# Kernel optimization log

Measured on AMD Instinct MI355X. Metric: run time of the kernel, lower is better.

The kernel has to match this reference:

```python
import jax, jax.numpy as jnp
import numpy as np

HEADS = 4
DIM_HEAD = 32
DIM = 128
EPS = 1e-12  # F.normalize eps


def _rmsnorm(t, g):
    # F.normalize over channel dim (dim=1), then * g * sqrt(dim)
    n = jnp.sqrt(jnp.sum(t * t, axis=1, keepdims=True))
    return t / jnp.maximum(n, EPS) * g * (DIM ** 0.5)


def setup_inputs() -> dict:
    key = jax.random.key(0)
    ks = jax.random.split(key, 5)
    b, H, W = 16, 96, 96
    x = jax.random.normal(ks[0], (b, DIM, H, W), dtype=jnp.float32)
    norm_g = jnp.ones((1, DIM, 1, 1), dtype=jnp.float32)
    qkv_w = jax.random.normal(ks[1], (3 * HEADS * DIM_HEAD, DIM), dtype=jnp.float32) * 0.05
    mem_kv = jax.random.normal(ks[2], (2, HEADS, DIM_HEAD, 4), dtype=jnp.float32)
    out_w = jax.random.normal(ks[3], (DIM, HEADS * DIM_HEAD), dtype=jnp.float32) * 0.05
    out_b = jnp.zeros((DIM,), dtype=jnp.float32)
    out_norm_g = jnp.ones((1, DIM, 1, 1), dtype=jnp.float32)
    return {"x": x, "norm_g": norm_g, "qkv_w": qkv_w, "mem_kv": mem_kv,
            "out_w": out_w, "out_b": out_b, "out_norm_g": out_norm_g}


def reference(x, norm_g, qkv_w, mem_kv, out_w, out_b, out_norm_g):
    b, c, H, W = x.shape
    n = H * W
    scale = DIM_HEAD ** (-0.5)

    xn = _rmsnorm(x, norm_g)
    # 1x1 conv (no bias) == channel GEMM
    qkv = jnp.einsum('oc,bchw->bohw', qkv_w, xn)  # [b, 3*h*d, H, W]
    q, k, v = jnp.split(qkv, 3, axis=1)

    def to_heads(t):
        return t.reshape(b, HEADS, DIM_HEAD, n)  # b h d n

    q, k, v = to_heads(q), to_heads(k), to_heads(v)

    mk = jnp.broadcast_to(mem_kv[0], (b, HEADS, DIM_HEAD, mem_kv.shape[-1]))
    mv = jnp.broadcast_to(mem_kv[1], (b, HEADS, DIM_HEAD, mem_kv.shape[-1]))
    k = jnp.concatenate([mk, k], axis=-1)
    v = jnp.concatenate([mv, v], axis=-1)

    q = jax.nn.softmax(q, axis=-2) * scale  # softmax over d
    k = jax.nn.softmax(k, axis=-1)          # softmax over n

    context = jnp.einsum('bhdn,bhen->bhde', k, v)  # [b,h,d,d]
    out = jnp.einsum('bhde,bhdn->bhen', context, q)  # [b,h,d,n]
    out = out.reshape(b, HEADS * DIM_HEAD, H, W)

    out = jnp.einsum('oc,bchw->bohw', out_w, out) + out_b[None, :, None, None]
    return _rmsnorm(out, out_norm_g)
```

## Files before the change

### kernel.cpp

```cpp
#include <hip/hip_runtime.h>
#include <hip/hip_bf16.h>
#include <math.h>

#define NPIX 9216
#define NBLK 48
#define TPB 6
#define NTILE 288
#define SCALE 0.17677669529663687f
#define SQRT128 11.313708498984761f

typedef __attribute__((ext_vector_type(8))) short short8;
typedef __attribute__((ext_vector_type(4))) float f32x4;

static __device__ __forceinline__ unsigned short f2bf(float f) {
  return __bfloat16_as_ushort(__float2bfloat16(f));
}
static __device__ __forceinline__ float bf2f(unsigned short h) {
  return __bfloat162float(__ushort_as_bfloat16(h));
}



__global__ __launch_bounds__(256) void k_prep2(
    const float* __restrict__ qkv_w, const float* __restrict__ norm_g,
    const float* __restrict__ out_w,
    unsigned short* __restrict__ wbf2, unsigned short* __restrict__ owb2) {
  const int i = blockIdx.x * 256 + threadIdx.x;
  if (i < 6144) {
    const int g = i >> 6, lane = i & 63;
    const int wv = g / 24, rem = g % 24;
    const int mt = rem >> 2, ks = rem & 3;
    const int row = (mt >> 1) * 128 + wv * 32 + (mt & 1) * 16 + (lane & 15);
    const int col = ks * 32 + (lane >> 4) * 8;
    const float* src = qkv_w + row * 128 + col;
    const float* gg = norm_g + col;
    uint4 o;
    o.x = (unsigned)f2bf(src[0] * gg[0]) | ((unsigned)f2bf(src[1] * gg[1]) << 16);
    o.y = (unsigned)f2bf(src[2] * gg[2]) | ((unsigned)f2bf(src[3] * gg[3]) << 16);
    o.z = (unsigned)f2bf(src[4] * gg[4]) | ((unsigned)f2bf(src[5] * gg[5]) << 16);
    o.w = (unsigned)f2bf(src[6] * gg[6]) | ((unsigned)f2bf(src[7] * gg[7]) << 16);
    *(uint4*)(wbf2 + (size_t)i * 8) = o;
  } else if (i < 8192) {
    const int i2 = i - 6144;
    const int g = i2 >> 6, lane = i2 & 63;
    const int wv = g >> 3, rem = g & 7;
    const int mt = rem >> 2, ks = rem & 3;
    const int row = 32 * wv + mt * 16 + (lane & 15);
    const int col = ks * 32 + (lane >> 4) * 8;
    const float* src = out_w + row * 128 + col;
    uint4 o;
    o.x = (unsigned)f2bf(src[0]) | ((unsigned)f2bf(src[1]) << 16);
    o.y = (unsigned)f2bf(src[2]) | ((unsigned)f2bf(src[3]) << 16);
    o.z = (unsigned)f2bf(src[4]) | ((unsigned)f2bf(src[5]) << 16);
    o.w = (unsigned)f2bf(src[6]) | ((unsigned)f2bf(src[7]) << 16);
    *(uint4*)(owb2 + (size_t)i2 * 8) = o;
  }
}

__global__ __launch_bounds__(256) void k_init(const float* __restrict__ mem_kv,
                                              float* __restrict__ ctxG,
                                              float* __restrict__ sumexpG) {
  const int bh = blockIdx.x;
  const int h = bh & 3;
  const float* mk = mem_kv + h * 128;
  const float* mv = mem_kv + 512 + h * 128;
  const int t = threadIdx.x;
  const int d = t >> 3, e0 = (t & 7) * 4;
  float ek[4], se = 0.f;
#pragma unroll
  for (int j = 0; j < 4; ++j) { ek[j] = __expf(mk[d * 4 + j]); se += ek[j]; }
#pragma unroll
  for (int ei = 0; ei < 4; ++ei) {
    const int e = e0 + ei;
    float s = 0.f;
#pragma unroll
    for (int j = 0; j < 4; ++j) s += ek[j] * mv[e * 4 + j];
    ctxG[(bh * 32 + d) * 32 + e] = s;
  }
  if ((t & 7) == 0) sumexpG[bh * 32 + d] = se;
}

template <bool WSQ>
__global__ __launch_bounds__(256, 3) void k1(
    const float* __restrict__ x, const unsigned short* __restrict__ wbf2,
    unsigned short* __restrict__ qb16, float* __restrict__ qf32,
    float* __restrict__ ctx_dst, float* __restrict__ se_dst) {
  __shared__ __align__(16) unsigned char smem[20480 + 17408 + 4096];
  unsigned short* kv = (unsigned short*)smem;
  unsigned short* xnT0 = (unsigned short*)(smem + 20480);
  float* redu0 = (float*)(smem + 20480 + 17408);

  const int t = threadIdx.x;
  const int b = blockIdx.y;
  const int blk = blockIdx.x;
  const int wv = t >> 6;
  const int lane = t & 63;
  const int lr = lane & 15;
  const int lg = lane >> 4;
  const int r = t >> 3, c4 = (t & 7) * 4;
  const float* xb = x + ((size_t)b * 128) * NPIX + blk * TPB * 32;
  unsigned short* kv_w = kv + wv * 64 * 40;

  f32x4 ctx[2][2];
#pragma unroll
  for (int i = 0; i < 2; ++i)
#pragma unroll
    for (int j = 0; j < 2; ++j)
#pragma unroll
      for (int q = 0; q < 4; ++q) ctx[i][j][q] = 0.f;
  float se_row[2] = {0.f, 0.f};

  float4 pf[4];
#pragma unroll
  for (int pass = 0; pass < 4; ++pass)
    pf[pass] = *(const float4*)(xb + (size_t)(pass * 32 + r) * NPIX + c4);

  for (int it = 0; it < TPB; ++it) {
    const int tile = blk * TPB + it;
    unsigned short* xnT = xnT0 + (it & 1) * 4352;
    float* redu = redu0 + (it & 1) * 512;

    {
      float ss0 = 0.f, ss1 = 0.f, ss2 = 0.f, ss3 = 0.f;
#pragma unroll
      for (int pass = 0; pass < 4; ++pass) {
        const int row = pass * 32 + r;
        const float4 v = pf[pass];
        xnT[(c4 + 0) * 136 + row] = f2bf(v.x);
        xnT[(c4 + 1) * 136 + row] = f2bf(v.y);
        xnT[(c4 + 2) * 136 + row] = f2bf(v.z);
        xnT[(c4 + 3) * 136 + row] = f2bf(v.w);
        ss0 = fmaf(v.x, v.x, ss0); ss1 = fmaf(v.y, v.y, ss1);
        ss2 = fmaf(v.z, v.z, ss2); ss3 = fmaf(v.w, v.w, ss3);
      }
      ss0 += __shfl_xor(ss0, 8); ss1 += __shfl_xor(ss1, 8);
      ss2 += __shfl_xor(ss2, 8); ss3 += __shfl_xor(ss3, 8);
      if (!(t & 8))
        *(float4*)&redu[(t >> 4) * 32 + c4] = make_float4(ss0, ss1, ss2, ss3);
    }
    __syncthreads();
    float iv0, iv1;
    {
      float invv = 0.f;
      if (lane < 32) {
        float s = 0.f;
#pragma unroll
        for (int g = 0; g < 16; ++g) s += redu[g * 32 + lane];
        invv = SQRT128 / fmaxf(sqrtf(s), 1e-12f);
      }
      iv0 = __shfl(invv, lr);
      iv1 = __shfl(invv, 16 + lr);
    }
    short8 bfr[4][2];
#pragma unroll
    for (int ks = 0; ks < 4; ++ks)
#pragma unroll
      for (int nt = 0; nt < 2; ++nt)
        bfr[ks][nt] = *(const short8*)&xnT[(nt * 16 + lr) * 136 + ks * 32 + lg * 8];
    if (it + 1 < TPB) {
      const float* xb2 = xb + (it + 1) * 32;
#pragma unroll
      for (int pass = 0; pass < 4; ++pass)
        pf[pass] = *(const float4*)(xb2 + (size_t)(pass * 32 + r) * NPIX + c4);
    }
    const unsigned short* wbase = wbf2 + (size_t)(wv * 24) * 512 + lane * 8;
    {
      f32x4 aq[2][2];
#pragma unroll
      for (int i = 0; i < 2; ++i)
#pragma unroll
        for (int j = 0; j < 2; ++j)
#pragma unroll
          for (int q = 0; q < 4; ++q) aq[i][j][q] = 0.f;
#pragma unroll
      for (int mt = 0; mt < 2; ++mt)
#pragma unroll
        for (int ks = 0; ks < 4; ++ks) {
          const short8 af = *(const short8*)(wbase + (size_t)(mt * 4 + ks) * 512);
          aq[mt][0] = __builtin_amdgcn_mfma_f32_16x16x32_bf16(af, bfr[ks][0], aq[mt][0], 0, 0, 0);
          aq[mt][1] = __builtin_amdgcn_mfma_f32_16x16x32_bf16(af, bfr[ks][1], aq[mt][1], 0, 0, 0);
        }
#pragma unroll
      for (int nt = 0; nt < 2; ++nt) {
        const float iv = nt ? iv1 : iv0;
        float qv[8];
#pragma unroll
        for (int j = 0; j < 8; ++j) qv[j] = aq[j >> 2][nt][j & 3] * iv;
        float m = qv[0];
#pragma unroll
        for (int j = 1; j < 8; ++j) m = fmaxf(m, qv[j]);
        m = fmaxf(m, __shfl_xor(m, 16));
        m = fmaxf(m, __shfl_xor(m, 32));
        float s = 0.f;
#pragma unroll
        for (int j = 0; j < 8; ++j) { qv[j] = __expf(qv[j] - m); s += qv[j]; }
        s += __shfl_xor(s, 16);
        s += __shfl_xor(s, 32);
        const float rs = SCALE / s;
        if (WSQ) {
          uint4 qo;
          qo.x = (unsigned)f2bf(qv[0] * rs) | ((unsigned)f2bf(qv[1] * rs) << 16);
          qo.y = (unsigned)f2bf(qv[2] * rs) | ((unsigned)f2bf(qv[3] * rs) << 16);
          qo.z = (unsigned)f2bf(qv[4] * rs) | ((unsigned)f2bf(qv[5] * rs) << 16);
          qo.w = (unsigned)f2bf(qv[6] * rs) | ((unsigned)f2bf(qv[7] * rs) << 16);
          *(uint4*)(qb16 +
              ((((size_t)(b * NTILE + tile) * 4 + wv) * 2 + nt) * 64 + lane) * 8) = qo;
        } else {
#pragma unroll
          for (int j = 0; j < 8; ++j) {
            const int d = (j >> 2) * 16 + lg * 4 + (j & 3);
            qf32[((size_t)b * 128 + wv * 32 + d) * NPIX + tile * 32 + nt * 16 + lr] = qv[j] * rs;
          }
        }
      }
    }
    {
#pragma unroll 2
      for (int mt = 2; mt < 6; ++mt) {
        f32x4 a0 = {0.f, 0.f, 0.f, 0.f};
        f32x4 a1 = {0.f, 0.f, 0.f, 0.f};
#pragma unroll
        for (int ks = 0; ks < 4; ++ks) {
          const short8 af = *(const short8*)(wbase + (size_t)(mt * 4 + ks) * 512);
          a0 = __builtin_amdgcn_mfma_f32_16x16x32_bf16(af, bfr[ks][0], a0, 0, 0, 0);
          a1 = __builtin_amdgcn_mfma_f32_16x16x32_bf16(af, bfr[ks][1], a1, 0, 0, 0);
        }
#pragma unroll
        for (int q = 0; q < 4; ++q) {
          const int row_l = (mt - 2) * 16 + lg * 4 + q;
          const unsigned pk = (unsigned)f2bf(a0[q] * iv0)
                            | ((unsigned)f2bf(a1[q] * iv1) << 16);
          *(unsigned*)&kv_w[row_l * 40 + lr * 2] = pk;
        }
      }
    }
    {
      short8 afk[2];
#pragma unroll
      for (int dt = 0; dt < 2; ++dt) {
        const short8 kraw = *(const short8*)&kv_w[(dt * 16 + lr) * 40 + lg * 8];
        short8 e16;
        float s = 0.f;
#pragma unroll
        for (int j = 0; j < 8; ++j) {
          const float ev = __expf(bf2f((unsigned short)kraw[j]));
          e16[j] = (short)f2bf(ev);
          s += ev;
        }
        afk[dt] = e16;
        s += __shfl_xor(s, 16);
        s += __shfl_xor(s, 32);
        se_row[dt] += s;
      }
#pragma unroll
      for (int dt = 0; dt < 2; ++dt)
#pragma unroll
        for (int et = 0; et < 2; ++et) {
          const short8 bf = *(const short8*)&kv_w[(32 + et * 16 + lr) * 40 + lg * 8];
          ctx[dt][et] = __builtin_amdgcn_mfma_f32_16x16x32_bf16(afk[dt], bf, ctx[dt][et], 0, 0, 0);
        }
    }
  }

  if (WSQ) {
    float* dst = ctx_dst + ((size_t)(b * NBLK + blk)) * 4096 + wv * 1024;
#pragma unroll
    for (int dt = 0; dt < 2; ++dt)
#pragma unroll
      for (int et = 0; et < 2; ++et)
#pragma unroll
        for (int q = 0; q < 4; ++q)
          dst[(dt * 16 + lg * 4 + q) * 32 + et * 16 + lr] = ctx[dt][et][q];
    if (lg == 0) {
#pragma unroll
      for (int dt = 0; dt < 2; ++dt)
        se_dst[(b * NBLK + blk) * 128 + wv * 32 + dt * 16 + lr] = se_row[dt];
    }
  } else {
#pragma unroll
    for (int dt = 0; dt < 2; ++dt)
#pragma unroll
      for (int et = 0; et < 2; ++et)
#pragma unroll
        for (int q = 0; q < 4; ++q)
          atomicAdd(&ctx_dst[((size_t)b * 128 + wv * 32 + dt * 16 + lg * 4 + q) * 32 + et * 16 + lr],
                    ctx[dt][et][q]);
    if (lg == 0) {
#pragma unroll
      for (int dt = 0; dt < 2; ++dt)
        atomicAdd(&se_dst[b * 128 + wv * 32 + dt * 16 + lr], se_row[dt]);
    }
  }
}

__global__ __launch_bounds__(256) void k_reduce(
    const float* __restrict__ part_ctx, const float* __restrict__ part_se,
    const float* __restrict__ mem_kv, unsigned short* __restrict__ ctxnT) {
  const int bid = blockIdx.x;
  const int b = bid >> 4, h = (bid >> 2) & 3, dq = bid & 3;
  const int t = threadIdx.x;
  const int dd = t >> 5;
  const int d = dq * 8 + dd;
  const int e = t & 31;
  __shared__ float sise[8];

  const float* mk = mem_kv + h * 128 + d * 4;
  const float* mv = mem_kv + 512 + h * 128 + e * 4;
  float ek[4];
  float acc = 0.f;
#pragma unroll
  for (int j = 0; j < 4; ++j) ek[j] = __expf(mk[j]);
#pragma unroll
  for (int j = 0; j < 4; ++j) acc += ek[j] * mv[j];
  const float* src = part_ctx + (size_t)b * NBLK * 4096 + h * 1024 + d * 32 + e;
  for (int p = 0; p < NBLK; ++p) acc += src[(size_t)p * 4096];
  if (e == 0) {
    float se = ek[0] + ek[1] + ek[2] + ek[3];
    const float* sp = part_se + (size_t)b * NBLK * 128 + h * 32 + d;
    for (int p = 0; p < NBLK; ++p) se += sp[(size_t)p * 128];
    sise[dd] = 1.f / se;
  }
  __syncthreads();
  const int c = ((d >> 2) & 3) * 8 + ((d >> 4) & 1) * 4 + (d & 3);
  ctxnT[(size_t)(b * 4 + h) * 1024 + e * 32 + c] = f2bf(acc * sise[dd]);
}

__global__ __launch_bounds__(256) void k_norm(
    const float* __restrict__ ctxG, const float* __restrict__ seG,
    unsigned short* __restrict__ ctxnT) {
  const int b = blockIdx.x;
  const int t = threadIdx.x;
  const int h = t >> 6, d = (t >> 1) & 31, e0 = (t & 1) * 16;
  const int r = h * 32 + d;
  const float ise = 1.f / seG[b * 128 + r];
  const float* src = ctxG + ((size_t)b * 128 + r) * 32;
  unsigned short* dst = ctxnT + ((size_t)(b * 4 + h) * 32) * 32;
  const int c = ((d >> 2) & 3) * 8 + ((d >> 4) & 1) * 4 + (d & 3);
#pragma unroll
  for (int i = 0; i < 16; ++i)
    dst[(e0 + i) * 32 + c] = f2bf(src[e0 + i] * ise);
}

__global__ __launch_bounds__(256) void k3_ws(
    const unsigned short* __restrict__ ctxnT, const unsigned short* __restrict__ owb2,
    const unsigned short* __restrict__ qbf, const float* __restrict__ out_b,
    const float* __restrict__ out_norm_g, float* __restrict__ out) {
  __shared__ __align__(16) unsigned char smem[8704 + 2048 + 128];
  unsigned short* o1T = (unsigned short*)smem;
  float* redu = (float*)(smem + 8704);
  float* inv = (float*)(smem + 8704 + 2048);

  const int t = threadIdx.x;
  const int b = blockIdx.y;
  const int tile = blockIdx.x;
  const int p0 = tile * 32;
  const int wv = t >> 6;
  const int lane = t & 63;
  const int lr = lane & 15;
  const int lg = lane >> 4;

  {
    f32x4 o1a[2][2];
#pragma unroll
    for (int i = 0; i < 2; ++i)
#pragma unroll
      for (int j = 0; j < 2; ++j)
#pragma unroll
        for (int q = 0; q < 4; ++q) o1a[i][j][q] = 0.f;
    const unsigned short* cbase = ctxnT + (size_t)(b * 4 + wv) * 1024;
    const unsigned short* qb = qbf + (((size_t)(b * NTILE + tile) * 4 + wv) * 2) * 512;
    short8 bq[2];
#pragma unroll
    for (int nt = 0; nt < 2; ++nt)
      bq[nt] = *(const short8*)(qb + (size_t)(nt * 64 + lane) * 8);
#pragma unroll
    for (int mt = 0; mt < 2; ++mt) {
      const short8 af = *(const short8*)(cbase + (mt * 16 + lr) * 32 + lg * 8);
#pragma unroll
      for (int nt = 0; nt < 2; ++nt)
        o1a[mt][nt] = __builtin_amdgcn_mfma_f32_16x16x32_bf16(af, bq[nt], o1a[mt][nt], 0, 0, 0);
    }
#pragma unroll
    for (int mt = 0; mt < 2; ++mt)
#pragma unroll
      for (int nt = 0; nt < 2; ++nt)
#pragma unroll
        for (int q = 0; q < 4; ++q) {
          const int e = wv * 32 + mt * 16 + lg * 4 + q;
          o1T[(nt * 16 + lr) * 136 + e] = f2bf(o1a[mt][nt][q]);
        }
  }
  __syncthreads();
  f32x4 y[2][2];
#pragma unroll
  for (int i = 0; i < 2; ++i)
#pragma unroll
    for (int j = 0; j < 2; ++j)
#pragma unroll
      for (int q = 0; q < 4; ++q) y[i][j][q] = 0.f;
  const unsigned short* wbase = owb2 + (size_t)(wv * 8) * 512 + lane * 8;
#pragma unroll
  for (int mt = 0; mt < 2; ++mt) {
#pragma unroll
    for (int ks = 0; ks < 4; ++ks) {
      const short8 af = *(const short8*)(wbase + (size_t)(mt * 4 + ks) * 512);
#pragma unroll
      for (int nt = 0; nt < 2; ++nt) {
        const short8 bf = *(const short8*)&o1T[(nt * 16 + lr) * 136 + ks * 32 + lg * 8];
        y[mt][nt] = __builtin_amdgcn_mfma_f32_16x16x32_bf16(af, bf, y[mt][nt], 0, 0, 0);
      }
    }
  }
  {
    float ss[2] = {0.f, 0.f};
#pragma unroll
    for (int mt = 0; mt < 2; ++mt)
#pragma unroll
      for (int q = 0; q < 4; ++q) {
        const int row = 32 * wv + mt * 16 + lg * 4 + q;
        const float bb = out_b[row];
#pragma unroll
        for (int nt = 0; nt < 2; ++nt) {
          y[mt][nt][q] += bb;
          ss[nt] = fmaf(y[mt][nt][q], y[mt][nt][q], ss[nt]);
        }
      }
#pragma unroll
    for (int nt = 0; nt < 2; ++nt)
      redu[(wv * 4 + lg) * 32 + nt * 16 + lr] = ss[nt];
  }
  __syncthreads();
  if (t < 32) {
    float s = 0.f;
#pragma unroll
    for (int g = 0; g < 16; ++g) s += redu[g * 32 + t];
    inv[t] = SQRT128 / fmaxf(sqrtf(s), 1e-12f);
  }
  __syncthreads();
  {
    float* ob = out + (size_t)b * 128 * NPIX + p0;
#pragma unroll
    for (int mt = 0; mt < 2; ++mt)
#pragma unroll
      for (int q = 0; q < 4; ++q) {
        const int row = 32 * wv + mt * 16 + lg * 4 + q;
        const float g = out_norm_g[row];
#pragma unroll
        for (int nt = 0; nt < 2; ++nt) {
          const int col = nt * 16 + lr;
          ob[(size_t)row * NPIX + col] = y[mt][nt][q] * inv[col] * g;
        }
      }
  }
}

__global__ __launch_bounds__(256) void k3f(
    const unsigned short* __restrict__ ctxnT, const unsigned short* __restrict__ owb2,
    const float* __restrict__ out_b, const float* __restrict__ out_norm_g,
    float* __restrict__ io) {
  __shared__ __align__(16) unsigned char smem[8704 + 8704 + 2048 + 128];
  unsigned short* qT = (unsigned short*)smem;
  unsigned short* o1T = (unsigned short*)(smem + 8704);
  float* redu = (float*)(smem + 8704 + 8704);
  float* inv = (float*)(smem + 8704 + 8704 + 2048);

  const int t = threadIdx.x;
  const int b = blockIdx.y;
  const int p0 = blockIdx.x * 32;
  const int wv = t >> 6;
  const int lane = t & 63;
  const int lr = lane & 15;
  const int lg = lane >> 4;

  {
    const float* qb = io + (size_t)b * 128 * NPIX + p0;
    const int r = t >> 3, c4 = (t & 7) * 4;
#pragma unroll
    for (int pass = 0; pass < 4; ++pass) {
      const int row = pass * 32 + r;
      const int dl = row & 31;
      const int pc = (row & ~31) | (((dl >> 2) & 3) * 8 + ((dl >> 4) & 1) * 4 + (dl & 3));
      const float4 v = *(const float4*)(qb + (size_t)row * NPIX + c4);
      qT[(c4 + 0) * 136 + pc] = f2bf(v.x);
      qT[(c4 + 1) * 136 + pc] = f2bf(v.y);
      qT[(c4 + 2) * 136 + pc] = f2bf(v.z);
      qT[(c4 + 3) * 136 + pc] = f2bf(v.w);
    }
  }
  __syncthreads();
  {
    f32x4 o1a[2][2];
#pragma unroll
    for (int i = 0; i < 2; ++i)
#pragma unroll
      for (int j = 0; j < 2; ++j)
#pragma unroll
        for (int q = 0; q < 4; ++q) o1a[i][j][q] = 0.f;
    const unsigned short* cbase = ctxnT + (size_t)(b * 4 + wv) * 1024;
#pragma unroll
    for (int mt = 0; mt < 2; ++mt) {
      const short8 af = *(const short8*)(cbase + (mt * 16 + lr) * 32 + lg * 8);
#pragma unroll
      for (int nt = 0; nt < 2; ++nt) {
        const short8 bf = *(const short8*)&qT[(nt * 16 + lr) * 136 + wv * 32 + lg * 8];
        o1a[mt][nt] = __builtin_amdgcn_mfma_f32_16x16x32_bf16(af, bf, o1a[mt][nt], 0, 0, 0);
      }
    }
#pragma unroll
    for (int mt = 0; mt < 2; ++mt)
#pragma unroll
      for (int nt = 0; nt < 2; ++nt)
#pragma unroll
        for (int q = 0; q < 4; ++q) {
          const int e = wv * 32 + mt * 16 + lg * 4 + q;
          o1T[(nt * 16 + lr) * 136 + e] = f2bf(o1a[mt][nt][q]);
        }
  }
  __syncthreads();
  f32x4 y[2][2];
#pragma unroll
  for (int i = 0; i < 2; ++i)
#pragma unroll
    for (int j = 0; j < 2; ++j)
#pragma unroll
      for (int q = 0; q < 4; ++q) y[i][j][q] = 0.f;
  const unsigned short* wbase = owb2 + (size_t)(wv * 8) * 512 + lane * 8;
#pragma unroll
  for (int mt = 0; mt < 2; ++mt) {
#pragma unroll
    for (int ks = 0; ks < 4; ++ks) {
      const short8 af = *(const short8*)(wbase + (size_t)(mt * 4 + ks) * 512);
#pragma unroll
      for (int nt = 0; nt < 2; ++nt) {
        const short8 bf = *(const short8*)&o1T[(nt * 16 + lr) * 136 + ks * 32 + lg * 8];
        y[mt][nt] = __builtin_amdgcn_mfma_f32_16x16x32_bf16(af, bf, y[mt][nt], 0, 0, 0);
      }
    }
  }
  {
    float ss[2] = {0.f, 0.f};
#pragma unroll
    for (int mt = 0; mt < 2; ++mt)
#pragma unroll
      for (int q = 0; q < 4; ++q) {
        const int row = 32 * wv + mt * 16 + lg * 4 + q;
        const float bb = out_b[row];
#pragma unroll
        for (int nt = 0; nt < 2; ++nt) {
          y[mt][nt][q] += bb;
          ss[nt] = fmaf(y[mt][nt][q], y[mt][nt][q], ss[nt]);
        }
      }
#pragma unroll
    for (int nt = 0; nt < 2; ++nt)
      redu[(wv * 4 + lg) * 32 + nt * 16 + lr] = ss[nt];
  }
  __syncthreads();
  if (t < 32) {
    float s = 0.f;
#pragma unroll
    for (int g = 0; g < 16; ++g) s += redu[g * 32 + t];
    inv[t] = SQRT128 / fmaxf(sqrtf(s), 1e-12f);
  }
  __syncthreads();
  {
    float* ob = io + (size_t)b * 128 * NPIX + p0;
#pragma unroll
    for (int mt = 0; mt < 2; ++mt)
#pragma unroll
      for (int q = 0; q < 4; ++q) {
        const int row = 32 * wv + mt * 16 + lg * 4 + q;
        const float g = out_norm_g[row];
#pragma unroll
        for (int nt = 0; nt < 2; ++nt) {
          const int col = nt * 16 + lr;
          ob[(size_t)row * NPIX + col] = y[mt][nt][q] * inv[col] * g;
        }
      }
  }
}

extern "C" void kernel_launch(void* const* d_in, const int* in_sizes, int n_in,
                              void* d_out, int out_size, void* d_ws, size_t ws_size,
                              hipStream_t stream) {
  const float* x          = (const float*)d_in[0];
  const float* norm_g     = (const float*)d_in[1];
  const float* qkv_w      = (const float*)d_in[2];
  const float* mem_kv     = (const float*)d_in[3];
  const float* out_w      = (const float*)d_in[4];
  const float* out_b      = (const float*)d_in[5];
  const float* out_norm_g = (const float*)d_in[6];
  float* out = (float*)d_out;

  const size_t PC = (size_t)16 * NBLK * 4096;
  const size_t PS = (size_t)16 * NBLK * 128;
  const size_t QB = (size_t)16 * NPIX * 128;
  const size_t need = (PC + PS) * 4 + (49152 + 16384 + 65536 + QB) * 2;

  if (ws_size >= need) {
    float* part_ctx = (float*)d_ws;
    float* part_se  = part_ctx + PC;
    unsigned short* wbf2  = (unsigned short*)(part_se + PS);
    unsigned short* owb2  = wbf2 + 49152;
    unsigned short* ctxnT = owb2 + 16384;
    unsigned short* qbf   = ctxnT + 65536;
    k_prep2<<<32, 256, 0, stream>>>(qkv_w, norm_g, out_w, wbf2, owb2);
    k1<true><<<dim3(NBLK, 16), 256, 0, stream>>>(x, wbf2, qbf, nullptr, part_ctx, part_se);
    k_reduce<<<256, 256, 0, stream>>>(part_ctx, part_se, mem_kv, ctxnT);
    k3_ws<<<dim3(NTILE, 16), 256, 0, stream>>>(ctxnT, owb2, qbf, out_b, out_norm_g, out);
  } else {
    float* ctxG = (float*)d_ws;
    float* seG  = ctxG + 65536;
    unsigned short* wbf2  = (unsigned short*)(seG + 2048);
    unsigned short* owb2  = wbf2 + 49152;
    unsigned short* ctxnT = owb2 + 16384;
    k_prep2<<<32, 256, 0, stream>>>(qkv_w, norm_g, out_w, wbf2, owb2);
    k_init<<<64, 256, 0, stream>>>(mem_kv, ctxG, seG);
    k1<false><<<dim3(NBLK, 16), 256, 0, stream>>>(x, wbf2, nullptr, out, ctxG, seG);
    k_norm<<<16, 256, 0, stream>>>(ctxG, seG, ctxnT);
    k3f<<<dim3(NTILE, 16), 256, 0, stream>>>(ctxnT, owb2, out_b, out_norm_g, out);
  }
}
```

Baseline: 72.81 us.

## Process 64-pixel tiles per iteration in k1 with uneven block partition

The first kernel now handles 64 pixels per loop iteration instead of 32. Each weight fragment load therefore feeds four MFMA column tiles instead of two, and the grid drops from 48 to 32 blocks per batch, with the 144 64-pixel tiles split 5/4 across blocks. The double-buffered xnT/redu staging is replaced by a single buffer plus an extra barrier. The q-softmax max subtraction is dropped, on the assumption that the normalized values are bounded. The cost is more registers and LDS, occupancy lowered to 2 blocks per SM, and a possible overflow risk in exp without the max shift.

```diff
diff --git a/kernel.cpp b/kernel.cpp
--- a/kernel.cpp
+++ b/kernel.cpp
@@ -3,8 +3,7 @@
 #include <math.h>
 
 #define NPIX 9216
-#define NBLK 48
-#define TPB 6
+#define NBLK 32
 #define NTILE 288
 #define SCALE 0.17677669529663687f
 #define SQRT128 11.313708498984761f
@@ -81,14 +80,14 @@
 }
 
 template <bool WSQ>
-__global__ __launch_bounds__(256, 3) void k1(
+__global__ __launch_bounds__(256, 2) void k1(
     const float* __restrict__ x, const unsigned short* __restrict__ wbf2,
     unsigned short* __restrict__ qb16, float* __restrict__ qf32,
     float* __restrict__ ctx_dst, float* __restrict__ se_dst) {
-  __shared__ __align__(16) unsigned char smem[20480 + 17408 + 4096];
+  __shared__ __align__(16) unsigned char smem[36864 + 17408 + 4096];
   unsigned short* kv = (unsigned short*)smem;
-  unsigned short* xnT0 = (unsigned short*)(smem + 20480);
-  float* redu0 = (float*)(smem + 20480 + 17408);
+  unsigned short* xnT = (unsigned short*)(smem + 36864);
+  float* redu = (float*)(smem + 36864 + 17408);
 
   const int t = threadIdx.x;
   const int b = blockIdx.y;
@@ -98,8 +97,11 @@
   const int lr = lane & 15;
   const int lg = lane >> 4;
   const int r = t >> 3, c4 = (t & 7) * 4;
-  const float* xb = x + ((size_t)b * 128) * NPIX + blk * TPB * 32;
-  unsigned short* kv_w = kv + wv * 64 * 40;
+  const float* xb = x + ((size_t)b * 128) * NPIX;
+  unsigned short* kv_w = kv + wv * 64 * 72;
+
+  const int tstart = (blk < 16) ? blk * 5 : 80 + (blk - 16) * 4;
+  const int tcnt = (blk < 16) ? 5 : 4;
 
   f32x4 ctx[2][2];
 #pragma unroll
@@ -110,66 +112,78 @@
       for (int q = 0; q < 4; ++q) ctx[i][j][q] = 0.f;
   float se_row[2] = {0.f, 0.f};
 
-  float4 pf[4];
+  float4 pf[8];
 #pragma unroll
   for (int pass = 0; pass < 4; ++pass)
-    pf[pass] = *(const float4*)(xb + (size_t)(pass * 32 + r) * NPIX + c4);
-
-  for (int it = 0; it < TPB; ++it) {
-    const int tile = blk * TPB + it;
-    unsigned short* xnT = xnT0 + (it & 1) * 4352;
-    float* redu = redu0 + (it & 1) * 512;
+#pragma unroll
+    for (int hf = 0; hf < 2; ++hf)
+      pf[pass * 2 + hf] = *(const float4*)(
+          xb + (size_t)(pass * 32 + r) * NPIX + tstart * 64 + hf * 32 + c4);
+
+  for (int it = 0; it < tcnt; ++it) {
+    const int T = tstart + it;
 
     {
-      float ss0 = 0.f, ss1 = 0.f, ss2 = 0.f, ss3 = 0.f;
-#pragma unroll
-      for (int pass = 0; pass < 4; ++pass) {
-        const int row = pass * 32 + r;
-        const float4 v = pf[pass];
-        xnT[(c4 + 0) * 136 + row] = f2bf(v.x);
-        xnT[(c4 + 1) * 136 + row] = f2bf(v.y);
-        xnT[(c4 + 2) * 136 + row] = f2bf(v.z);
-        xnT[(c4 + 3) * 136 + row] = f2bf(v.w);
-        ss0 = fmaf(v.x, v.x, ss0); ss1 = fmaf(v.y, v.y, ss1);
-        ss2 = fmaf(v.z, v.z, ss2); ss3 = fmaf(v.w, v.w, ss3);
-      }
-      ss0 += __shfl_xor(ss0, 8); ss1 += __shfl_xor(ss1, 8);
-      ss2 += __shfl_xor(ss2, 8); ss3 += __shfl_xor(ss3, 8);
-      if (!(t & 8))
-        *(float4*)&redu[(t >> 4) * 32 + c4] = make_float4(ss0, ss1, ss2, ss3);
+      float ss[8];
+#pragma unroll
+      for (int i = 0; i < 8; ++i) ss[i] = 0.f;
+#pragma unroll
+      for (int pass = 0; pass < 4; ++pass)
+#pragma unroll
+        for (int hf = 0; hf < 2; ++hf) {
+          const int row = pass * 32 + r;
+          const int px0 = hf * 32 + c4;
+          const float4 v = pf[pass * 2 + hf];
+          xnT[(px0 + 0) * 136 + row] = f2bf(v.x);
+          xnT[(px0 + 1) * 136 + row] = f2bf(v.y);
+          xnT[(px0 + 2) * 136 + row] = f2bf(v.z);
+          xnT[(px0 + 3) * 136 + row] = f2bf(v.w);
+          ss[hf * 4 + 0] = fmaf(v.x, v.x, ss[hf * 4 + 0]);
+          ss[hf * 4 + 1] = fmaf(v.y, v.y, ss[hf * 4 + 1]);
+          ss[hf * 4 + 2] = fmaf(v.z, v.z, ss[hf * 4 + 2]);
+          ss[hf * 4 + 3] = fmaf(v.w, v.w, ss[hf * 4 + 3]);
+        }
+#pragma unroll
+      for (int i = 0; i < 8; ++i) ss[i] += __shfl_xor(ss[i], 8);
+      if (!(t & 8)) {
+        *(float4*)&redu[(t >> 4) * 64 + c4] =
+            make_float4(ss[0], ss[1], ss[2], ss[3]);
+        *(float4*)&redu[(t >> 4) * 64 + 32 + c4] =
+            make_float4(ss[4], ss[5], ss[6], ss[7]);
+      }
     }
     __syncthreads();
-    float iv0, iv1;
+    float iv[4];
     {
-      float invv = 0.f;
-      if (lane < 32) {
-        float s = 0.f;
-#pragma unroll
-        for (int g = 0; g < 16; ++g) s += redu[g * 32 + lane];
-        invv = SQRT128 / fmaxf(sqrtf(s), 1e-12f);
-      }
-      iv0 = __shfl(invv, lr);
-      iv1 = __shfl(invv, 16 + lr);
-    }
-    short8 bfr[4][2];
+      float s = 0.f;
+#pragma unroll
+      for (int g = 0; g < 16; ++g) s += redu[g * 64 + lane];
+      const float invv = SQRT128 / fmaxf(sqrtf(s), 1e-12f);
+#pragma unroll
+      for (int nt = 0; nt < 4; ++nt) iv[nt] = __shfl(invv, nt * 16 + lr);
+    }
+    short8 bfr[4][4];
 #pragma unroll
     for (int ks = 0; ks < 4; ++ks)
 #pragma unroll
-      for (int nt = 0; nt < 2; ++nt)
+      for (int nt = 0; nt < 4; ++nt)
         bfr[ks][nt] = *(const short8*)&xnT[(nt * 16 + lr) * 136 + ks * 32 + lg * 8];
-    if (it + 1 < TPB) {
-      const float* xb2 = xb + (it + 1) * 32;
+    if (it + 1 < tcnt) {
 #pragma unroll
       for (int pass = 0; pass < 4; ++pass)
-        pf[pass] = *(const float4*)(xb2 + (size_t)(pass * 32 + r) * NPIX + c4);
-    }
+#pragma unroll
+        for (int hf = 0; hf < 2; ++hf)
+          pf[pass * 2 + hf] = *(const float4*)(
+              xb + (size_t)(pass * 32 + r) * NPIX + (T + 1) * 64 + hf * 32 + c4);
+    }
+    __syncthreads();
     const unsigned short* wbase = wbf2 + (size_t)(wv * 24) * 512 + lane * 8;
     {
-      f32x4 aq[2][2];
+      f32x4 aq[2][4];
 #pragma unroll
       for (int i = 0; i < 2; ++i)
 #pragma unroll
-        for (int j = 0; j < 2; ++j)
+        for (int j = 0; j < 4; ++j)
 #pragma unroll
           for (int q = 0; q < 4; ++q) aq[i][j][q] = 0.f;
 #pragma unroll
@@ -177,26 +191,22 @@
 #pragma unroll
         for (int ks = 0; ks < 4; ++ks) {
           const short8 af = *(const short8*)(wbase + (size_t)(mt * 4 + ks) * 512);
-          aq[mt][0] = __builtin_amdgcn_mfma_f32_16x16x32_bf16(af, bfr[ks][0], aq[mt][0], 0, 0, 0);
-          aq[mt][1] = __builtin_amdgcn_mfma_f32_16x16x32_bf16(af, bfr[ks][1], aq[mt][1], 0, 0, 0);
-        }
-#pragma unroll
-      for (int nt = 0; nt < 2; ++nt) {
-        const float iv = nt ? iv1 : iv0;
+#pragma unroll
+          for (int nt = 0; nt < 4; ++nt)
+            aq[mt][nt] = __builtin_amdgcn_mfma_f32_16x16x32_bf16(af, bfr[ks][nt], aq[mt][nt], 0, 0, 0);
+        }
+#pragma unroll
+      for (int nt = 0; nt < 4; ++nt) {
         float qv[8];
 #pragma unroll
-        for (int j = 0; j < 8; ++j) qv[j] = aq[j >> 2][nt][j & 3] * iv;
-        float m = qv[0];
-#pragma unroll
-        for (int j = 1; j < 8; ++j) m = fmaxf(m, qv[j]);
-        m = fmaxf(m, __shfl_xor(m, 16));
-        m = fmaxf(m, __shfl_xor(m, 32));
+        for (int j = 0; j < 8; ++j) qv[j] = aq[j >> 2][nt][j & 3] * iv[nt];
         float s = 0.f;
 #pragma unroll
-        for (int j = 0; j < 8; ++j) { qv[j] = __expf(qv[j] - m); s += qv[j]; }
+        for (int j = 0; j < 8; ++j) { qv[j] = __expf(qv[j]); s += qv[j]; }
         s += __shfl_xor(s, 16);
         s += __shfl_xor(s, 32);
         const float rs = SCALE / s;
+        const int tile32 = T * 2 + (nt >> 1);
         if (WSQ) {
           uint4 qo;
           qo.x = (unsigned)f2bf(qv[0] * rs) | ((unsigned)f2bf(qv[1] * rs) << 16);
@@ -204,50 +214,58 @@
           qo.z = (unsigned)f2bf(qv[4] * rs) | ((unsigned)f2bf(qv[5] * rs) << 16);
           qo.w = (unsigned)f2bf(qv[6] * rs) | ((unsigned)f2bf(qv[7] * rs) << 16);
           *(uint4*)(qb16 +
-              ((((size_t)(b * NTILE + tile) * 4 + wv) * 2 + nt) * 64 + lane) * 8) = qo;
+              ((((size_t)(b * NTILE + tile32) * 4 + wv) * 2 + (nt & 1)) * 64 + lane) * 8) = qo;
         } else {
 #pragma unroll
           for (int j = 0; j < 8; ++j) {
             const int d = (j >> 2) * 16 + lg * 4 + (j & 3);
-            qf32[((size_t)b * 128 + wv * 32 + d) * NPIX + tile * 32 + nt * 16 + lr] = qv[j] * rs;
+            qf32[((size_t)b * 128 + wv * 32 + d) * NPIX + tile32 * 32 + (nt & 1) * 16 + lr] = qv[j] * rs;
           }
         }
       }
     }
     {
-#pragma unroll 2
+#pragma unroll
       for (int mt = 2; mt < 6; ++mt) {
-        f32x4 a0 = {0.f, 0.f, 0.f, 0.f};
-        f32x4 a1 = {0.f, 0.f, 0.f, 0.f};
+        f32x4 a[4];
+#pragma unroll
+        for (int j = 0; j < 4; ++j) a[j] = (f32x4){0.f, 0.f, 0.f, 0.f};
 #pragma unroll
         for (int ks = 0; ks < 4; ++ks) {
           const short8 af = *(const short8*)(wbase + (size_t)(mt * 4 + ks) * 512);
-          a0 = __builtin_amdgcn_mfma_f32_16x16x32_bf16(af, bfr[ks][0], a0, 0, 0, 0);
-          a1 = __builtin_amdgcn_mfma_f32_16x16x32_bf16(af, bfr[ks][1], a1, 0, 0, 0);
+#pragma unroll
+          for (int nt = 0; nt < 4; ++nt)
+            a[nt] = __builtin_amdgcn_mfma_f32_16x16x32_bf16(af, bfr[ks][nt], a[nt], 0, 0, 0);
         }
 #pragma unroll
         for (int q = 0; q < 4; ++q) {
           const int row_l = (mt - 2) * 16 + lg * 4 + q;
-          const unsigned pk = (unsigned)f2bf(a0[q] * iv0)
-                            | ((unsigned)f2bf(a1[q] * iv1) << 16);
-          *(unsigned*)&kv_w[row_l * 40 + lr * 2] = pk;
+          const unsigned pk01 = (unsigned)f2bf(a[0][q] * iv[0])
+                              | ((unsigned)f2bf(a[1][q] * iv[1]) << 16);
+          const unsigned pk23 = (unsigned)f2bf(a[2][q] * iv[2])
+                              | ((unsigned)f2bf(a[3][q] * iv[3]) << 16);
+          *(unsigned*)&kv_w[row_l * 72 + lr * 2] = pk01;
+          *(unsigned*)&kv_w[row_l * 72 + 32 + lr * 2] = pk23;
         }
       }
     }
     {
-      short8 afk[2];
+      short8 afk[2][2];
 #pragma unroll
       for (int dt = 0; dt < 2; ++dt) {
-        const short8 kraw = *(const short8*)&kv_w[(dt * 16 + lr) * 40 + lg * 8];
-        short8 e16;
         float s = 0.f;
 #pragma unroll
-        for (int j = 0; j < 8; ++j) {
-          const float ev = __expf(bf2f((unsigned short)kraw[j]));
-          e16[j] = (short)f2bf(ev);
-          s += ev;
-        }
-        afk[dt] = e16;
+        for (int hf = 0; hf < 2; ++hf) {
+          const short8 kraw = *(const short8*)&kv_w[(dt * 16 + lr) * 72 + hf * 32 + lg * 8];
+          short8 e16;
+#pragma unroll
+          for (int j = 0; j < 8; ++j) {
+            const float ev = __expf(bf2f((unsigned short)kraw[j]));
+            e16[j] = (short)f2bf(ev);
+            s += ev;
+          }
+          afk[dt][hf] = e16;
+        }
         s += __shfl_xor(s, 16);
         s += __shfl_xor(s, 32);
         se_row[dt] += s;
@@ -255,10 +273,12 @@
 #pragma unroll
       for (int dt = 0; dt < 2; ++dt)
 #pragma unroll
-        for (int et = 0; et < 2; ++et) {
-          const short8 bf = *(const short8*)&kv_w[(32 + et * 16 + lr) * 40 + lg * 8];
-          ctx[dt][et] = __builtin_amdgcn_mfma_f32_16x16x32_bf16(afk[dt], bf, ctx[dt][et], 0, 0, 0);
-        }
+        for (int et = 0; et < 2; ++et)
+#pragma unroll
+          for (int hf = 0; hf < 2; ++hf) {
+            const short8 bf = *(const short8*)&kv_w[(32 + et * 16 + lr) * 72 + hf * 32 + lg * 8];
+            ctx[dt][et] = __builtin_amdgcn_mfma_f32_16x16x32_bf16(afk[dt][hf], bf, ctx[dt][et], 0, 0, 0);
+          }
     }
   }
 
```

New measurement: 79.13 us. +8.7%, slower.
